# Optimization experiments

Measured on AMD Instinct MI355X. Metric: run time of the kernel, lower is better.

Reference implementation:

```python
import jax, jax.numpy as jnp
import numpy as np

N = 2048        # num_nodes
E = 32768       # num input edges (avg degree 16)
F = 8           # edge feature dim
E_MAX = 1_048_576  # static padding for output edge count (expected ~525K two-hop + 32K orig)


def setup_inputs() -> dict:
    key = jax.random.key(0)
    k1, k2, k3 = jax.random.split(key, 3)
    src = jax.random.randint(k1, (E,), 0, N, dtype=jnp.int32)
    dst = jax.random.randint(k2, (E,), 0, N, dtype=jnp.int32)
    edge_index = jnp.stack([src, dst])                     # [2, E]
    edge_attr = jax.random.normal(k3, (E, F), dtype=jnp.float32)
    return {"num_nodes": N, "edge_index": edge_index, "edge_attr": edge_attr}


def reference(num_nodes, edge_index, edge_attr):
    n = num_nodes
    f = edge_attr.shape[1]
    src, dst = edge_index[0], edge_index[1]

    # to_torch_coo_tensor: adjacency with ones. Dense stand-in for SpGEMM.
    A = jnp.zeros((n, n), jnp.float32).at[src, dst].set(1.0)   # presence (input assumed coalesced)
    A2 = A @ A                                                  # path counts; structure of adj @ adj

    # remove_self_loops on the two-hop edges
    mask2 = (A2 > 0) & (~jnp.eye(n, dtype=bool))

    # original edge mask
    orig = jnp.zeros((n, n), dtype=bool).at[src, dst].set(True)

    # coalesce: union of edge sets, sorted lexicographically by (row, col).
    combined = orig | mask2

    # coalesce reduce='sum': duplicates of original edges sum their attrs;
    # two-hop-only edges contribute zeros (edge_attr2 = new_zeros).
    attr_dense = jnp.zeros((n, n, f), edge_attr.dtype).at[src, dst].add(edge_attr)

    # row-major nonzero == lexicographic (row, col) sort; static size via padding.
    rows, cols = jnp.nonzero(combined, size=E_MAX, fill_value=0)
    count = combined.sum()
    valid = jnp.arange(E_MAX) < count

    out_edge_index = jnp.stack([
        jnp.where(valid, rows, -1),
        jnp.where(valid, cols, -1),
    ]).astype(jnp.int32)                                        # [2, E_MAX], -1 padded
    out_attr = attr_dense[rows, cols] * valid[:, None]          # [E_MAX, F], zero padded
    return out_edge_index, out_attr
```

## Files before the change

### kernel.cpp

```cpp
#include <hip/hip_runtime.h>

#define N_NODES 2048
#define WORDS   64
#define E_MAX_OUT 1048576
#define FDIM    8
#define EL_CAP  64


__global__ void k_init(float* __restrict__ out_attr, unsigned* __restrict__ a_bits,
                       int* __restrict__ ecnt) {
    int tid = blockIdx.x * blockDim.x + threadIdx.x;
    int nth = gridDim.x * blockDim.x;
    const int A4 = FDIM * E_MAX_OUT / 4;
    float4* o4 = (float4*)out_attr;
    for (int p = tid; p < A4; p += nth) o4[p] = make_float4(0.f, 0.f, 0.f, 0.f);
    uint4* a4 = (uint4*)a_bits;
    for (int p = tid; p < N_NODES * WORDS / 4; p += nth) a4[p] = make_uint4(0u, 0u, 0u, 0u);
    for (int p = tid; p < N_NODES; p += nth) ecnt[p] = 0;
}

__global__ void k_build(const int* __restrict__ ei, int E, unsigned* __restrict__ a_bits,
                        int* __restrict__ ecnt, int* __restrict__ elist) {
    int e = blockIdx.x * blockDim.x + threadIdx.x;
    if (e >= E) return;
    int s = ei[e];
    int d = ei[E + e];
    atomicOr(&a_bits[s * WORDS + (d >> 5)], 1u << (d & 31));
    int slot = atomicAdd(&ecnt[s], 1);
    if (slot < EL_CAP) elist[s * EL_CAP + slot] = e;
}

__global__ void __launch_bounds__(256) k_twohop(const unsigned* __restrict__ a_bits,
                                                unsigned* __restrict__ c_bits,
                                                int* __restrict__ rel_off,
                                                int* __restrict__ row_cnt) {
    int lane = threadIdx.x & 63;
    int wv   = threadIdx.x >> 6;
    int i    = blockIdx.x * 4 + wv;
    __shared__ int nbr[4][256];
    __shared__ int ncnt_sh[4];

    unsigned r = a_bits[i * WORDS + lane];
    int pc = __popc(r);
    int incl = pc;
    for (int off = 1; off < 64; off <<= 1) {
        int v = __shfl_up(incl, off, 64);
        if (lane >= off) incl += v;
    }
    int base = incl - pc;
    unsigned bits = r;
    int wb = lane << 5;
    while (bits) {
        int b = __ffs(bits) - 1;
        bits &= bits - 1;
        nbr[wv][base++] = wb + b;
    }
    if (lane == 63) ncnt_sh[wv] = incl;
    __syncthreads();

    int nc = ncnt_sh[wv];
    const int* nb = nbr[wv];
    unsigned acc = 0u;
    int j = 0;
    for (; j + 4 <= nc; j += 4) {
        unsigned x0 = a_bits[nb[j]     * WORDS + lane];
        unsigned x1 = a_bits[nb[j + 1] * WORDS + lane];
        unsigned x2 = a_bits[nb[j + 2] * WORDS + lane];
        unsigned x3 = a_bits[nb[j + 3] * WORDS + lane];
        acc |= (x0 | x1) | (x2 | x3);
    }
    for (; j < nc; ++j) acc |= a_bits[nb[j] * WORDS + lane];

    if (lane == (i >> 5)) acc &= ~(1u << (i & 31));
    acc |= r;
    c_bits[i * WORDS + lane] = acc;

    int cnt = __popc(acc);
    int incl2 = cnt;
    for (int off = 1; off < 64; off <<= 1) {
        int v = __shfl_up(incl2, off, 64);
        if (lane >= off) incl2 += v;
    }
    rel_off[i * WORDS + lane] = incl2 - cnt;
    if (lane == 63) row_cnt[i] = incl2;
}

__global__ void __launch_bounds__(128) k_emit_attr(const unsigned* __restrict__ c_bits,
                                                   const int* __restrict__ rel_off,
                                                   const int* __restrict__ row_cnt,
                                                   const int* __restrict__ ei,
                                                   const float* __restrict__ attr, int E,
                                                   const int* __restrict__ ecnt,
                                                   const int* __restrict__ elist,
                                                   float* __restrict__ out) {
    int i    = blockIdx.x;
    int t    = threadIdx.x;
    int lane = t & 63;
    int wave = t >> 6;
    __shared__ int sh_lt[2], sh_all[2];

    int p_lt = 0, p_all = 0;
    #pragma unroll
    for (int q = 0; q < N_NODES / 128; ++q) {
        int idx = t * (N_NODES / 128) + q;
        int v = row_cnt[idx];
        p_all += v;
        if (idx < i) p_lt += v;
    }
    for (int off = 32; off; off >>= 1) {
        p_lt  += __shfl_down(p_lt,  off, 64);
        p_all += __shfl_down(p_all, off, 64);
    }
    if (lane == 0) { sh_lt[wave] = p_lt; sh_all[wave] = p_all; }
    __syncthreads();
    int row_off_i = sh_lt[0] + sh_lt[1];
    int count     = sh_all[0] + sh_all[1];

    if (wave == 0) {
        unsigned c = c_bits[i * WORDS + lane];
        int p = row_off_i + rel_off[i * WORDS + lane];
        float fi = (float)i;
        int wb = lane << 5;
        while (c) {
            int b = __ffs(c) - 1;
            c &= c - 1;
            out[p]             = fi;
            out[E_MAX_OUT + p] = (float)(wb + b);
            ++p;
        }
    } else {
        float* oattr = out + 2 * E_MAX_OUT;
        int ne = ecnt[i];
        int q  = lane & 3;
        for (int slot = lane >> 2; slot < ne; slot += 16) {
            int e = elist[i * EL_CAP + slot];
            int d = ei[E + e];
            int dw = d >> 5;
            unsigned cw = c_bits[i * WORDS + dw];
            int p = row_off_i + rel_off[i * WORDS + dw]
                  + __popc(cw & ((1u << (d & 31)) - 1u));
            atomicAdd(&oattr[p * FDIM + 2 * q],     attr[e * FDIM + 2 * q]);
            atomicAdd(&oattr[p * FDIM + 2 * q + 1], attr[e * FDIM + 2 * q + 1]);
        }
    }

    long long P = (long long)(E_MAX_OUT - count);
    int s0 = count + (int)(P * i / N_NODES);
    int s1 = count + (int)(P * (i + 1) / N_NODES);
    for (int p = s0 + t; p < s1; p += 128) {
        out[p]             = -1.0f;
        out[E_MAX_OUT + p] = -1.0f;
    }
}

extern "C" void kernel_launch(void* const* d_in, const int* in_sizes, int n_in,
                              void* d_out, int out_size, void* d_ws, size_t ws_size,
                              hipStream_t stream) {
    const int*   ei   = (const int*)d_in[1];
    const float* attr = (const float*)d_in[2];
    int E = in_sizes[1] / 2;

    float* out = (float*)d_out;
    unsigned char* ws = (unsigned char*)d_ws;
    unsigned* a_bits  = (unsigned*)(ws);
    unsigned* c_bits  = (unsigned*)(ws + 512 * 1024);
    int*      rel_off = (int*)(ws + 1024 * 1024);
    int*      row_cnt = (int*)(ws + 1536 * 1024);
    int*      ecnt    = (int*)(ws + 1544 * 1024);
    int*      elist   = (int*)(ws + 1552 * 1024);

    k_init     <<<2048, 256, 0, stream>>>(out + 2 * E_MAX_OUT, a_bits, ecnt);
    k_build    <<<(E + 255) / 256, 256, 0, stream>>>(ei, E, a_bits, ecnt, elist);
    k_twohop   <<<N_NODES / 4, 256, 0, stream>>>(a_bits, c_bits, rel_off, row_cnt);
    k_emit_attr<<<N_NODES, 128, 0, stream>>>(c_bits, rel_off, row_cnt, ei, attr, E,
                                             ecnt, elist, out);
}
```

Before: 32.27 us.

## Write attributes densely per row instead of zero-fill plus atomic scatter

Drops the separate 32 MB zero-fill of the attribute output in the init kernel. The emit kernel now stages each row's original edges (destination and features) in shared memory. Every output slot of the row then computes its attribute sum by scanning those edges and writes it as float4s, and padding slots are zeroed in the same pass. This removes the write-then-atomic-add traffic on the large output, at the cost of a per-output linear scan over up to 64 staged edges and a re-read of the column index from global memory.

Measured after the change: 37.80 us. 1.17x slower.

```diff
diff --git a/kernel.cpp b/kernel.cpp
--- a/kernel.cpp
+++ b/kernel.cpp
@@ -7,16 +7,11 @@
 #define EL_CAP  64
 
 
-__global__ void k_init(float* __restrict__ out_attr, unsigned* __restrict__ a_bits,
-                       int* __restrict__ ecnt) {
-    int tid = blockIdx.x * blockDim.x + threadIdx.x;
-    int nth = gridDim.x * blockDim.x;
-    const int A4 = FDIM * E_MAX_OUT / 4;
-    float4* o4 = (float4*)out_attr;
-    for (int p = tid; p < A4; p += nth) o4[p] = make_float4(0.f, 0.f, 0.f, 0.f);
-    uint4* a4 = (uint4*)a_bits;
-    for (int p = tid; p < N_NODES * WORDS / 4; p += nth) a4[p] = make_uint4(0u, 0u, 0u, 0u);
-    for (int p = tid; p < N_NODES; p += nth) ecnt[p] = 0;
+__global__ void __launch_bounds__(256) k_init(unsigned* __restrict__ a_bits,
+                                              int* __restrict__ ecnt) {
+    int t = blockIdx.x * blockDim.x + threadIdx.x;
+    ((uint4*)a_bits)[t] = make_uint4(0u, 0u, 0u, 0u);
+    if (t < N_NODES) ecnt[t] = 0;
 }
 
 __global__ void k_build(const int* __restrict__ ei, int E, unsigned* __restrict__ a_bits,
@@ -85,24 +80,26 @@
     if (lane == 63) row_cnt[i] = incl2;
 }
 
-__global__ void __launch_bounds__(128) k_emit_attr(const unsigned* __restrict__ c_bits,
-                                                   const int* __restrict__ rel_off,
-                                                   const int* __restrict__ row_cnt,
-                                                   const int* __restrict__ ei,
-                                                   const float* __restrict__ attr, int E,
-                                                   const int* __restrict__ ecnt,
-                                                   const int* __restrict__ elist,
-                                                   float* __restrict__ out) {
+__global__ void __launch_bounds__(256) k_emit(const unsigned* __restrict__ c_bits,
+                                              const int* __restrict__ rel_off,
+                                              const int* __restrict__ row_cnt,
+                                              const int* __restrict__ ei,
+                                              const float* __restrict__ attr, int E,
+                                              const int* __restrict__ ecnt,
+                                              const int* __restrict__ elist,
+                                              float* __restrict__ out) {
     int i    = blockIdx.x;
     int t    = threadIdx.x;
     int lane = t & 63;
     int wave = t >> 6;
-    __shared__ int sh_lt[2], sh_all[2];
+    __shared__ int   sh_lt[4], sh_all[4];
+    __shared__ int   s_dst[EL_CAP];
+    __shared__ float s_attr[EL_CAP][FDIM];
 
     int p_lt = 0, p_all = 0;
     #pragma unroll
-    for (int q = 0; q < N_NODES / 128; ++q) {
-        int idx = t * (N_NODES / 128) + q;
+    for (int q = 0; q < N_NODES / 256; ++q) {
+        int idx = t * (N_NODES / 256) + q;
         int v = row_cnt[idx];
         p_all += v;
         if (idx < i) p_lt += v;
@@ -112,9 +109,20 @@
         p_all += __shfl_down(p_all, off, 64);
     }
     if (lane == 0) { sh_lt[wave] = p_lt; sh_all[wave] = p_all; }
+
+    int ne = ecnt[i];
+    if (ne > EL_CAP) ne = EL_CAP;
+    if (t < ne) {
+        int e = elist[i * EL_CAP + t];
+        s_dst[t] = ei[E + e];
+        float4 lo = ((const float4*)(attr + (size_t)e * FDIM))[0];
+        float4 hi = ((const float4*)(attr + (size_t)e * FDIM))[1];
+        ((float4*)s_attr[t])[0] = lo;
+        ((float4*)s_attr[t])[1] = hi;
+    }
     __syncthreads();
-    int row_off_i = sh_lt[0] + sh_lt[1];
-    int count     = sh_all[0] + sh_all[1];
+    int row_off_i = sh_lt[0] + sh_lt[1] + sh_lt[2] + sh_lt[3];
+    int count     = sh_all[0] + sh_all[1] + sh_all[2] + sh_all[3];
 
     if (wave == 0) {
         unsigned c = c_bits[i * WORDS + lane];
@@ -128,28 +136,39 @@
             out[E_MAX_OUT + p] = (float)(wb + b);
             ++p;
         }
-    } else {
-        float* oattr = out + 2 * E_MAX_OUT;
-        int ne = ecnt[i];
-        int q  = lane & 3;
-        for (int slot = lane >> 2; slot < ne; slot += 16) {
-            int e = elist[i * EL_CAP + slot];
-            int d = ei[E + e];
-            int dw = d >> 5;
-            unsigned cw = c_bits[i * WORDS + dw];
-            int p = row_off_i + rel_off[i * WORDS + dw]
-                  + __popc(cw & ((1u << (d & 31)) - 1u));
-            atomicAdd(&oattr[p * FDIM + 2 * q],     attr[e * FDIM + 2 * q]);
-            atomicAdd(&oattr[p * FDIM + 2 * q + 1], attr[e * FDIM + 2 * q + 1]);
+    }
+    __syncthreads();
+
+    int cnt_i = row_cnt[i];
+    float* oattr = out + 2 * E_MAX_OUT;
+    for (int j = t; j < cnt_i; j += 256) {
+        int p = row_off_i + j;
+        int col = (int)out[E_MAX_OUT + p];
+        float4 lo = make_float4(0.f, 0.f, 0.f, 0.f);
+        float4 hi = make_float4(0.f, 0.f, 0.f, 0.f);
+        for (int e = 0; e < ne; ++e) {
+            if (s_dst[e] == col) {
+                float4 alo = ((float4*)s_attr[e])[0];
+                float4 ahi = ((float4*)s_attr[e])[1];
+                lo.x += alo.x; lo.y += alo.y; lo.z += alo.z; lo.w += alo.w;
+                hi.x += ahi.x; hi.y += ahi.y; hi.z += ahi.z; hi.w += ahi.w;
+            }
         }
+        float4* dst = (float4*)(oattr + (size_t)p * FDIM);
+        dst[0] = lo;
+        dst[1] = hi;
     }
 
     long long P = (long long)(E_MAX_OUT - count);
     int s0 = count + (int)(P * i / N_NODES);
     int s1 = count + (int)(P * (i + 1) / N_NODES);
-    for (int p = s0 + t; p < s1; p += 128) {
+    float4 z4 = make_float4(0.f, 0.f, 0.f, 0.f);
+    for (int p = s0 + t; p < s1; p += 256) {
         out[p]             = -1.0f;
         out[E_MAX_OUT + p] = -1.0f;
+        float4* dst = (float4*)(oattr + (size_t)p * FDIM);
+        dst[0] = z4;
+        dst[1] = z4;
     }
 }
 
@@ -169,9 +188,9 @@
     int*      ecnt    = (int*)(ws + 1544 * 1024);
     int*      elist   = (int*)(ws + 1552 * 1024);
 
-    k_init     <<<2048, 256, 0, stream>>>(out + 2 * E_MAX_OUT, a_bits, ecnt);
-    k_build    <<<(E + 255) / 256, 256, 0, stream>>>(ei, E, a_bits, ecnt, elist);
-    k_twohop   <<<N_NODES / 4, 256, 0, stream>>>(a_bits, c_bits, rel_off, row_cnt);
-    k_emit_attr<<<N_NODES, 128, 0, stream>>>(c_bits, rel_off, row_cnt, ei, attr, E,
-                                             ecnt, elist, out);
+    k_init  <<<128, 256, 0, stream>>>(a_bits, ecnt);
+    k_build <<<(E + 255) / 256, 256, 0, stream>>>(ei, E, a_bits, ecnt, elist);
+    k_twohop<<<N_NODES / 4, 256, 0, stream>>>(a_bits, c_bits, rel_off, row_cnt);
+    k_emit  <<<N_NODES, 256, 0, stream>>>(c_bits, rel_off, row_cnt, ei, attr, E,
+                                          ecnt, elist, out);
 }
```
